# Optimization experiments

Measured on AMD Instinct MI355X. Metric: run time of the kernel, lower is better.

The kernel has to match this reference:

```python
import jax, jax.numpy as jnp
import numpy as np

H = 256
W = 256
TANFOVX = 0.5
TANFOVY = 0.5
FX = W / (2.0 * TANFOVX)   # focal in pixels
FY = H / (2.0 * TANFOVY)
NEAR = 0.2                 # near-plane cull, as in 3DGS CUDA
COV_BLUR = 0.3             # low-pass added to 2D cov diagonal
P = 512


def quat_to_rot(q):
    # q: [P,4] (r,x,y,z) unnormalized -> [P,3,3]
    q = q / jnp.linalg.norm(q, axis=-1, keepdims=True)
    r, x, y, z = q[:, 0], q[:, 1], q[:, 2], q[:, 3]
    R = jnp.stack([
        1 - 2 * (y * y + z * z), 2 * (x * y - r * z), 2 * (x * z + r * y),
        2 * (x * y + r * z), 1 - 2 * (x * x + z * z), 2 * (y * z - r * x),
        2 * (x * z - r * y), 2 * (y * z + r * x), 1 - 2 * (x * x + y * y)],
        axis=-1).reshape(-1, 3, 3)
    return R


def setup_inputs() -> dict:
    key = jax.random.key(0)
    k = jax.random.split(key, 6)
    xy = jax.random.normal(k[0], (P, 2), dtype=jnp.float32) * 1.5
    z = jax.random.uniform(k[1], (P, 1), dtype=jnp.float32, minval=2.0, maxval=10.0)
    means3D = jnp.concatenate([xy, z], axis=1)                       # in front of camera
    scales = 0.02 + 0.15 * jax.random.uniform(k[2], (P, 3), dtype=jnp.float32)
    rotations = jax.random.normal(k[3], (P, 4), dtype=jnp.float32)
    opacities = jax.random.uniform(k[4], (P, 1), dtype=jnp.float32, minval=0.1, maxval=1.0)
    colors_precomp = jax.random.uniform(k[5], (P, 3), dtype=jnp.float32)
    viewmatrix = jnp.eye(4, dtype=jnp.float32)                       # camera at origin, +z forward
    zn, zf = 0.01, 100.0
    projmatrix = jnp.array([
        [1.0 / TANFOVX, 0.0, 0.0, 0.0],
        [0.0, 1.0 / TANFOVY, 0.0, 0.0],
        [0.0, 0.0, zf / (zf - zn), -(zf * zn) / (zf - zn)],
        [0.0, 0.0, 1.0, 0.0]], dtype=jnp.float32)                    # full proj (view = I)
    campos = jnp.zeros((3,), dtype=jnp.float32)
    bg = jnp.zeros((3,), dtype=jnp.float32)
    return {"means3D": means3D, "scales": scales, "rotations": rotations,
            "opacities": opacities, "colors_precomp": colors_precomp,
            "viewmatrix": viewmatrix, "projmatrix": projmatrix,
            "campos": campos, "bg": bg}


def reference(means3D, scales, rotations, opacities, colors_precomp,
              viewmatrix, projmatrix, campos, bg):
    n = means3D.shape[0]
    Rw = viewmatrix[:3, :3]
    p_view = means3D @ Rw.T + viewmatrix[:3, 3]                      # [P,3] camera space
    depth = p_view[:, 2]
    ones = jnp.ones((n, 1), means3D.dtype)
    p_hom = jnp.concatenate([means3D, ones], axis=1) @ projmatrix.T  # [P,4]
    pw = 1.0 / (p_hom[:, 3] + 1e-7)
    p_proj = p_hom[:, :3] * pw[:, None]                              # NDC
    # 3D covariance from scale + rotation: Sigma = (R S)(R S)^T
    R = quat_to_rot(rotations)
    M = R * scales[:, None, :]
    cov3d = M @ jnp.swapaxes(M, 1, 2)                                # [P,3,3]
    # EWA splatting Jacobian -> 2D covariance
    tz = jnp.where(jnp.abs(depth) < 1e-6, 1e-6, depth)
    limx, limy = 1.3 * TANFOVX, 1.3 * TANFOVY
    tx = jnp.clip(p_view[:, 0] / tz, -limx, limx) * tz
    ty = jnp.clip(p_view[:, 1] / tz, -limy, limy) * tz
    zero = jnp.zeros_like(tz)
    J = jnp.stack([FX / tz, zero, -FX * tx / (tz * tz),
                   zero, FY / tz, -FY * ty / (tz * tz)], axis=-1).reshape(-1, 2, 3)
    T = J @ Rw                                                        # [P,2,3]
    cov2d = T @ cov3d @ jnp.swapaxes(T, 1, 2)                         # [P,2,2]
    a = cov2d[:, 0, 0] + COV_BLUR
    b = cov2d[:, 0, 1]
    c = cov2d[:, 1, 1] + COV_BLUR
    det = a * c - b * b
    valid = (depth > NEAR) & (det > 0.0)
    det_s = jnp.where(valid, det, 1.0)
    conic_a, conic_b, conic_c = c / det_s, -b / det_s, a / det_s
    mid = 0.5 * (a + c)
    lam = mid + jnp.sqrt(jnp.maximum(mid * mid - det, 0.1))
    radii = jnp.where(valid, jnp.ceil(3.0 * jnp.sqrt(lam)), 0.0).astype(jnp.int32)
    # NDC -> pixel centers
    px = ((p_proj[:, 0] + 1.0) * W - 1.0) * 0.5
    py = ((p_proj[:, 1] + 1.0) * H - 1.0) * 0.5
    # global front-to-back depth sort (replaces per-tile radix sort)
    order = jnp.argsort(depth)
    px, py = px[order], py[order]
    ca, cb, cc = conic_a[order], conic_b[order], conic_c[order]
    op = opacities[order, 0]
    col = colors_precomp[order]
    dep = depth[order]
    vmask = valid[order]
    ys, xs = jnp.meshgrid(jnp.arange(H, dtype=means3D.dtype),
                          jnp.arange(W, dtype=means3D.dtype), indexing='ij')
    xs, ys = xs.reshape(-1), ys.reshape(-1)                           # [HW]
    dx = px[:, None] - xs[None, :]                                    # [P,HW]
    dy = py[:, None] - ys[None, :]
    power = -0.5 * (ca[:, None] * dx * dx + cc[:, None] * dy * dy) - cb[:, None] * dx * dy
    alpha = jnp.minimum(0.99, op[:, None] * jnp.exp(power))
    keep = (power <= 0.0) & (alpha >= 1.0 / 255.0) & vmask[:, None]
    alpha = jnp.where(keep, alpha, 0.0)
    Tcum = jnp.cumprod(1.0 - alpha, axis=0)                           # transmittance after each gaussian
    T_excl = jnp.concatenate([jnp.ones((1, alpha.shape[1]), alpha.dtype), Tcum[:-1]], axis=0)
    wgt = alpha * T_excl                                              # compositing weights [P,HW]
    Tfin = Tcum[-1]
    color = jnp.einsum('ph,pc->ch', wgt, col) + Tfin[None, :] * bg[:, None]
    depth_map = jnp.einsum('ph,p->h', wgt, dep)
    opac_map = 1.0 - Tfin
    n_touched = jnp.zeros((n,), jnp.int32).at[order].set(
        jnp.sum(keep, axis=1).astype(jnp.int32))
    return (color.reshape(3, H, W), radii, depth_map.reshape(H, W),
            opac_map.reshape(H, W), n_touched)
```

## Files before the change

### kernel.cpp

```cpp
#include <hip/hip_runtime.h>

constexpr int   P     = 512;
constexpr int   W     = 256;
constexpr int   H     = 256;
constexpr float FXc   = 256.0f;
constexpr float FYc   = 256.0f;
constexpr float NEARc = 0.2f;
constexpr float BLUR  = 0.3f;
constexpr float LIMX  = 0.65f;
constexpr float LIMY  = 0.65f;

constexpr int COLOR_OFF = 0;
constexpr int RADII_OFF = 196608;
constexpr int DEPTH_OFF = 197120;
constexpr int OPAC_OFF  = 262656;
constexpr int NT_OFF    = 328192;

__global__ __launch_bounds__(256, 4) void fused_q_kernel(
    const float* __restrict__ means3D, const float* __restrict__ scales,
    const float* __restrict__ rots,    const float* __restrict__ opacs,
    const float* __restrict__ cols,    const float* __restrict__ vm,
    const float* __restrict__ pm,      const float* __restrict__ bg,
    float* __restrict__ out)
{
    __shared__ float4 g4u[P * 3];
    __shared__ float  sdep[P];
    __shared__ int    sorig[P];
    __shared__ int    rank2slot[P + 1];
    __shared__ float  part[3][5][64];
    __shared__ float4 ntrec[2];
    __shared__ int    s_cnt;
    __shared__ int    s_n;

    const int tid   = threadIdx.x;
    const int bid   = blockIdx.x;
    const int row   = bid >> 2;
    const int xbase = (bid & 3) * 64;
    const int wv    = tid >> 6;
    const int lane  = tid & 63;
    const float fy  = (float)row;

    if (tid == 0) { s_n = 0; s_cnt = 0; }
    __syncthreads();

    #pragma unroll
    for (int k = 0; k < 2; ++k) {
        const int g = tid + k * 256;

        const float mx = means3D[g*3+0], my = means3D[g*3+1], mz = means3D[g*3+2];

        const float pv0 = vm[0]*mx + vm[1]*my + vm[2]*mz  + vm[3];
        const float pv1 = vm[4]*mx + vm[5]*my + vm[6]*mz  + vm[7];
        const float pv2 = vm[8]*mx + vm[9]*my + vm[10]*mz + vm[11];
        const float depth = pv2;

        const float ph0 = pm[0]*mx  + pm[1]*my  + pm[2]*mz  + pm[3];
        const float ph1 = pm[4]*mx  + pm[5]*my  + pm[6]*mz  + pm[7];
        const float ph3 = pm[12]*mx + pm[13]*my + pm[14]*mz + pm[15];
        const float pwn = 1.0f / (ph3 + 1e-7f);
        const float pp0 = ph0 * pwn, pp1 = ph1 * pwn;

        float q0 = rots[g*4+0], q1 = rots[g*4+1], q2 = rots[g*4+2], q3 = rots[g*4+3];
        const float qinv = 1.0f / sqrtf(q0*q0 + q1*q1 + q2*q2 + q3*q3);
        q0 *= qinv; q1 *= qinv; q2 *= qinv; q3 *= qinv;
        const float r = q0, x = q1, y = q2, z = q3;
        const float R00 = 1.f - 2.f*(y*y + z*z), R01 = 2.f*(x*y - r*z), R02 = 2.f*(x*z + r*y);
        const float R10 = 2.f*(x*y + r*z), R11 = 1.f - 2.f*(x*x + z*z), R12 = 2.f*(y*z - r*x);
        const float R20 = 2.f*(x*z - r*y), R21 = 2.f*(y*z + r*x), R22 = 1.f - 2.f*(x*x + y*y);

        const float s0 = scales[g*3+0], s1 = scales[g*3+1], s2 = scales[g*3+2];
        const float M00 = R00*s0, M01 = R01*s1, M02 = R02*s2;
        const float M10 = R10*s0, M11 = R11*s1, M12 = R12*s2;
        const float M20 = R20*s0, M21 = R21*s1, M22 = R22*s2;
        const float c00 = M00*M00 + M01*M01 + M02*M02;
        const float c01 = M00*M10 + M01*M11 + M02*M12;
        const float c02 = M00*M20 + M01*M21 + M02*M22;
        const float c11 = M10*M10 + M11*M11 + M12*M12;
        const float c12 = M10*M20 + M11*M21 + M12*M22;
        const float c22 = M20*M20 + M21*M21 + M22*M22;

        const float tz  = (fabsf(depth) < 1e-6f) ? 1e-6f : depth;
        const float txc = fminf(fmaxf(pv0 / tz, -LIMX), LIMX) * tz;
        const float tyc = fminf(fmaxf(pv1 / tz, -LIMY), LIMY) * tz;

        const float J00 = FXc / tz, J02 = -FXc * txc / (tz*tz);
        const float J11 = FYc / tz, J12 = -FYc * tyc / (tz*tz);

        const float T00 = J00*vm[0] + J02*vm[8];
        const float T01 = J00*vm[1] + J02*vm[9];
        const float T02 = J00*vm[2] + J02*vm[10];
        const float T10 = J11*vm[4] + J12*vm[8];
        const float T11 = J11*vm[5] + J12*vm[9];
        const float T12 = J11*vm[6] + J12*vm[10];

        const float V00 = T00*c00 + T01*c01 + T02*c02;
        const float V01 = T00*c01 + T01*c11 + T02*c12;
        const float V02 = T00*c02 + T01*c12 + T02*c22;
        const float V10 = T10*c00 + T11*c01 + T12*c02;
        const float V11 = T10*c01 + T11*c11 + T12*c12;
        const float V12 = T10*c02 + T11*c12 + T12*c22;

        const float a = V00*T00 + V01*T01 + V02*T02 + BLUR;
        const float b = V00*T10 + V01*T11 + V02*T12;
        const float c = V10*T10 + V11*T11 + V12*T12 + BLUR;
        const float det = a*c - b*b;

        const bool  valid = (depth > NEARc) && (det > 0.0f);
        const float det_s = valid ? det : 1.0f;
        const float conic_a =  c / det_s;
        const float conic_b = -b / det_s;
        const float conic_c =  a / det_s;

        const float op = opacs[g];
        const float L  = logf(255.0f * op);
        const float rowrad2 = valid ? (2.0f * c * L) * 1.0001f + 1e-4f : -1.0f;
        const float xrad2   = valid ? (2.0f * a * L) * 1.0001f + 1e-4f : -1.0f;

        if (bid == 0) {
            const float mid = 0.5f * (a + c);
            const float lam = mid + sqrtf(fmaxf(mid*mid - det, 0.1f));
            out[RADII_OFF + g] = valid ? ceilf(3.0f * sqrtf(lam)) : 0.0f;
        }

        const float px = ((pp0 + 1.0f) * (float)W - 1.0f) * 0.5f;
        const float py = ((pp1 + 1.0f) * (float)H - 1.0f) * 0.5f;

        if (g == bid) {
            ntrec[0] = make_float4(px, py, -0.5f * conic_a, -conic_b);
            ntrec[1] = make_float4(-0.5f * conic_c, op, xrad2, rowrad2);
        }

        const float dyv = py - fy;
        const float dxm = fmaxf(0.0f, fmaxf((float)xbase - px,
                                            px - (float)(xbase + 63)));
        if (dyv * dyv <= rowrad2 && dxm * dxm <= xrad2) {
            const int s = atomicAdd(&s_n, 1);
            g4u[s*3+0] = make_float4(py, -conic_b, px, -0.5f * conic_a);
            g4u[s*3+1] = make_float4(-0.5f * conic_c, op, depth, 0.0f);
            g4u[s*3+2] = make_float4(cols[g*3+0], cols[g*3+1], cols[g*3+2], 0.0f);
            sdep[s]  = depth;
            sorig[s] = g;
        }
    }
    __syncthreads();
    const int n = s_n;

    for (int t = tid; t < n; t += 256) {
        const float d = sdep[t];
        const int   o = sorig[t];
        int rank = 0;
        for (int j = 0; j < n; ++j) {
            const float dj = sdep[j];
            rank += (dj < d) || (dj == d && sorig[j] < o);
        }
        rank2slot[rank] = t;
    }
    __syncthreads();
    if (tid == 0) rank2slot[n] = (n > 0) ? rank2slot[n - 1] : 0;
    __syncthreads();

    const int beg = (n * wv) >> 2;
    const int end = (n * (wv + 1)) >> 2;
    const float fx = (float)(xbase + lane);
    float T = 1.0f, ar = 0.f, ag = 0.f, ab = 0.f, ad = 0.f;

    if (end > beg) {
        int slot = rank2slot[beg];
        float4 h  = g4u[slot*3+0];
        float4 mm = g4u[slot*3+1];
        float4 cl = g4u[slot*3+2];
        for (int t = beg; t < end; ++t) {
            const int sn = rank2slot[t + 1];
            const float4 hn  = g4u[sn*3+0];
            const float4 mmn = g4u[sn*3+1];
            const float4 cln = g4u[sn*3+2];

            const float dx = h.z - fx;
            const float dy = h.x - fy;
            const float pw = fmaf(h.w, dx*dx, fmaf(mm.x, dy*dy, h.y * dx * dy));
            const float alpha = fminf(0.99f, mm.y * __expf(pw));
            const bool keep = (pw <= 0.0f) && (alpha >= (1.0f / 255.0f));

            const float ae  = keep ? alpha : 0.0f;
            const float wgt = ae * T;
            ar = fmaf(wgt, cl.x, ar); ag = fmaf(wgt, cl.y, ag);
            ab = fmaf(wgt, cl.z, ab); ad = fmaf(wgt, mm.z, ad);
            T  = fmaf(-ae, T, T);

            h = hn; mm = mmn; cl = cln;
        }
    }

    if (wv > 0) {
        part[wv-1][0][lane] = ar; part[wv-1][1][lane] = ag;
        part[wv-1][2][lane] = ab; part[wv-1][3][lane] = ad;
        part[wv-1][4][lane] = T;
    }
    __syncthreads();
    if (wv == 0) {
        float fr = ar, fg = ag, fb = ab, fd = ad, fT = T;
        #pragma unroll
        for (int s = 0; s < 3; ++s) {
            fr = fmaf(fT, part[s][0][lane], fr);
            fg = fmaf(fT, part[s][1][lane], fg);
            fb = fmaf(fT, part[s][2][lane], fb);
            fd = fmaf(fT, part[s][3][lane], fd);
            fT *= part[s][4][lane];
        }
        const int pix = row * W + xbase + lane;
        out[COLOR_OFF + 0*65536 + pix] = fr + fT * bg[0];
        out[COLOR_OFF + 1*65536 + pix] = fg + fT * bg[1];
        out[COLOR_OFF + 2*65536 + pix] = fb + fT * bg[2];
        out[DEPTH_OFF + pix]           = fd;
        out[OPAC_OFF  + pix]           = 1.0f - fT;
    }

    if (bid < P) {
        const float4 r0 = ntrec[0], r1 = ntrec[1];
        const float pxg = r0.x, pyg = r0.y, pa = r0.z, pb = r0.w;
        const float pc = r1.x, opg = r1.y, rx2 = r1.z, ry2 = r1.w;
        int cc2 = 0;
        if (ry2 > 0.0f && rx2 > 0.0f) {
            const float ry = sqrtf(ry2), rx = sqrtf(rx2);
            const int y0 = max(0, (int)ceilf(pyg - ry));
            const int y1 = min(H - 1, (int)floorf(pyg + ry));
            const int x0 = max(0, (int)ceilf(pxg - rx));
            const int x1 = min(W - 1, (int)floorf(pxg + rx));
            const int xx = x0 + tid;
            if (xx <= x1 && y0 <= y1) {
                const float dx = (float)xx - pxg;
                const float padx2 = pa * dx * dx;
                for (int yy = y0; yy <= y1; ++yy) {
                    const float dy = (float)yy - pyg;
                    const float pw = fmaf(pc, dy*dy, fmaf(pb, dx*dy, padx2));
                    const float alpha = fminf(0.99f, opg * __expf(pw));
                    cc2 += (pw <= 0.0f) && (alpha >= (1.0f / 255.0f));
                }
            }
        }
        #pragma unroll
        for (int off = 32; off; off >>= 1) cc2 += __shfl_down(cc2, off);
        if (lane == 0 && cc2) atomicAdd(&s_cnt, cc2);
        __syncthreads();
        if (tid == 0) out[NT_OFF + bid] = (float)s_cnt;
    }
}

extern "C" void kernel_launch(void* const* d_in, const int* in_sizes, int n_in,
                              void* d_out, int out_size, void* d_ws, size_t ws_size,
                              hipStream_t stream) {
    const float* means3D = (const float*)d_in[0];
    const float* scales  = (const float*)d_in[1];
    const float* rots    = (const float*)d_in[2];
    const float* opacs   = (const float*)d_in[3];
    const float* cols    = (const float*)d_in[4];
    const float* vm      = (const float*)d_in[5];
    const float* pm      = (const float*)d_in[6];
    const float* bg      = (const float*)d_in[8];
    float* out = (float*)d_out;

    fused_q_kernel<<<4 * H, 256, 0, stream>>>(means3D, scales, rots, opacs,
                                              cols, vm, pm, bg, out);
}
```

Measured before the change: 20.57 us.

## Cull gaussians with cheap bound before full preprocessing; analytic n_touched row spans

Non-zero blocks first test each gaussian against a cheap conservative bound (max scale, depth, opacity) and run the full covariance/conic preprocessing only for the surviving candidates. Block 0 still preprocesses all gaussians to write radii. The n_touched count no longer loops over every row and evaluates exp per pixel: each thread takes one row and solves the conic quadratic to count the pixels inside the alpha threshold. This adds an extra barrier and candidate list, and the analytic count may differ from the per-pixel test at boundary pixels.

After: 17.18 us. 16.5% less time.

```diff
diff --git a/kernel.cpp b/kernel.cpp
--- a/kernel.cpp
+++ b/kernel.cpp
@@ -15,6 +15,98 @@
 constexpr int DEPTH_OFF = 197120;
 constexpr int OPAC_OFF  = 262656;
 constexpr int NT_OFF    = 328192;
+
+struct PrepR {
+    float px, py, pa, pb, pc, opv, depth;
+    float rr2, xr2;
+    float a, c, det, L;
+    bool  valid;
+};
+
+__device__ __forceinline__ PrepR full_prep(
+    int g,
+    const float* __restrict__ means3D, const float* __restrict__ scales,
+    const float* __restrict__ rots,    const float* __restrict__ opacs,
+    const float* __restrict__ vm,      const float* __restrict__ pm)
+{
+    PrepR o;
+    const float mx = means3D[g*3+0], my = means3D[g*3+1], mz = means3D[g*3+2];
+
+    const float pv0 = vm[0]*mx + vm[1]*my + vm[2]*mz  + vm[3];
+    const float pv1 = vm[4]*mx + vm[5]*my + vm[6]*mz  + vm[7];
+    const float pv2 = vm[8]*mx + vm[9]*my + vm[10]*mz + vm[11];
+    const float depth = pv2;
+
+    const float ph0 = pm[0]*mx  + pm[1]*my  + pm[2]*mz  + pm[3];
+    const float ph1 = pm[4]*mx  + pm[5]*my  + pm[6]*mz  + pm[7];
+    const float ph3 = pm[12]*mx + pm[13]*my + pm[14]*mz + pm[15];
+    const float pwn = 1.0f / (ph3 + 1e-7f);
+    const float pp0 = ph0 * pwn, pp1 = ph1 * pwn;
+
+    float q0 = rots[g*4+0], q1 = rots[g*4+1], q2 = rots[g*4+2], q3 = rots[g*4+3];
+    const float qinv = 1.0f / sqrtf(q0*q0 + q1*q1 + q2*q2 + q3*q3);
+    q0 *= qinv; q1 *= qinv; q2 *= qinv; q3 *= qinv;
+    const float r = q0, x = q1, y = q2, z = q3;
+    const float R00 = 1.f - 2.f*(y*y + z*z), R01 = 2.f*(x*y - r*z), R02 = 2.f*(x*z + r*y);
+    const float R10 = 2.f*(x*y + r*z), R11 = 1.f - 2.f*(x*x + z*z), R12 = 2.f*(y*z - r*x);
+    const float R20 = 2.f*(x*z - r*y), R21 = 2.f*(y*z + r*x), R22 = 1.f - 2.f*(x*x + y*y);
+
+    const float s0 = scales[g*3+0], s1 = scales[g*3+1], s2 = scales[g*3+2];
+    const float M00 = R00*s0, M01 = R01*s1, M02 = R02*s2;
+    const float M10 = R10*s0, M11 = R11*s1, M12 = R12*s2;
+    const float M20 = R20*s0, M21 = R21*s1, M22 = R22*s2;
+    const float c00 = M00*M00 + M01*M01 + M02*M02;
+    const float c01 = M00*M10 + M01*M11 + M02*M12;
+    const float c02 = M00*M20 + M01*M21 + M02*M22;
+    const float c11 = M10*M10 + M11*M11 + M12*M12;
+    const float c12 = M10*M20 + M11*M21 + M12*M22;
+    const float c22 = M20*M20 + M21*M21 + M22*M22;
+
+    const float tz  = (fabsf(depth) < 1e-6f) ? 1e-6f : depth;
+    const float txc = fminf(fmaxf(pv0 / tz, -LIMX), LIMX) * tz;
+    const float tyc = fminf(fmaxf(pv1 / tz, -LIMY), LIMY) * tz;
+
+    const float J00 = FXc / tz, J02 = -FXc * txc / (tz*tz);
+    const float J11 = FYc / tz, J12 = -FYc * tyc / (tz*tz);
+
+    const float T00 = J00*vm[0] + J02*vm[8];
+    const float T01 = J00*vm[1] + J02*vm[9];
+    const float T02 = J00*vm[2] + J02*vm[10];
+    const float T10 = J11*vm[4] + J12*vm[8];
+    const float T11 = J11*vm[5] + J12*vm[9];
+    const float T12 = J11*vm[6] + J12*vm[10];
+
+    const float V00 = T00*c00 + T01*c01 + T02*c02;
+    const float V01 = T00*c01 + T01*c11 + T02*c12;
+    const float V02 = T00*c02 + T01*c12 + T02*c22;
+    const float V10 = T10*c00 + T11*c01 + T12*c02;
+    const float V11 = T10*c01 + T11*c11 + T12*c12;
+    const float V12 = T10*c02 + T11*c12 + T12*c22;
+
+    const float a = V00*T00 + V01*T01 + V02*T02 + BLUR;
+    const float b = V00*T10 + V01*T11 + V02*T12;
+    const float c = V10*T10 + V11*T11 + V12*T12 + BLUR;
+    const float det = a*c - b*b;
+
+    const bool  valid = (depth > NEARc) && (det > 0.0f);
+    const float det_s = valid ? det : 1.0f;
+
+    o.pa = -0.5f * ( c / det_s);
+    o.pb = -(-b / det_s) * -1.0f;
+    o.pb = (b / det_s);
+    o.pc = -0.5f * ( a / det_s);
+    o.opv = opacs[g];
+    o.depth = depth;
+    const float L = logf(255.0f * o.opv);
+    o.L = L;
+    o.rr2 = valid ? (2.0f * c * L) * 1.0001f + 1e-4f : -1.0f;
+    o.xr2 = valid ? (2.0f * a * L) * 1.0001f + 1e-4f : -1.0f;
+    o.px = ((pp0 + 1.0f) * (float)W - 1.0f) * 0.5f;
+    o.py = ((pp1 + 1.0f) * (float)H - 1.0f) * 0.5f;
+    o.a = a; o.c = c; o.det = det;
+    o.valid = valid;
+    return o;
+}
 
 __global__ __launch_bounds__(256, 4) void fused_q_kernel(
     const float* __restrict__ means3D, const float* __restrict__ scales,
@@ -26,11 +118,11 @@
     __shared__ float4 g4u[P * 3];
     __shared__ float  sdep[P];
     __shared__ int    sorig[P];
+    __shared__ int    cand[P];
     __shared__ int    rank2slot[P + 1];
     __shared__ float  part[3][5][64];
     __shared__ float4 ntrec[2];
-    __shared__ int    s_cnt;
-    __shared__ int    s_n;
+    __shared__ int    s_cnt, s_n, s_ncand;
 
     const int tid   = threadIdx.x;
     const int bid   = blockIdx.x;
@@ -39,107 +131,79 @@
     const int wv    = tid >> 6;
     const int lane  = tid & 63;
     const float fy  = (float)row;
-
-    if (tid == 0) { s_n = 0; s_cnt = 0; }
-    __syncthreads();
-
-    #pragma unroll
-    for (int k = 0; k < 2; ++k) {
-        const int g = tid + k * 256;
-
-        const float mx = means3D[g*3+0], my = means3D[g*3+1], mz = means3D[g*3+2];
-
-        const float pv0 = vm[0]*mx + vm[1]*my + vm[2]*mz  + vm[3];
-        const float pv1 = vm[4]*mx + vm[5]*my + vm[6]*mz  + vm[7];
-        const float pv2 = vm[8]*mx + vm[9]*my + vm[10]*mz + vm[11];
-        const float depth = pv2;
-
-        const float ph0 = pm[0]*mx  + pm[1]*my  + pm[2]*mz  + pm[3];
-        const float ph1 = pm[4]*mx  + pm[5]*my  + pm[6]*mz  + pm[7];
-        const float ph3 = pm[12]*mx + pm[13]*my + pm[14]*mz + pm[15];
-        const float pwn = 1.0f / (ph3 + 1e-7f);
-        const float pp0 = ph0 * pwn, pp1 = ph1 * pwn;
-
-        float q0 = rots[g*4+0], q1 = rots[g*4+1], q2 = rots[g*4+2], q3 = rots[g*4+3];
-        const float qinv = 1.0f / sqrtf(q0*q0 + q1*q1 + q2*q2 + q3*q3);
-        q0 *= qinv; q1 *= qinv; q2 *= qinv; q3 *= qinv;
-        const float r = q0, x = q1, y = q2, z = q3;
-        const float R00 = 1.f - 2.f*(y*y + z*z), R01 = 2.f*(x*y - r*z), R02 = 2.f*(x*z + r*y);
-        const float R10 = 2.f*(x*y + r*z), R11 = 1.f - 2.f*(x*x + z*z), R12 = 2.f*(y*z - r*x);
-        const float R20 = 2.f*(x*z - r*y), R21 = 2.f*(y*z + r*x), R22 = 1.f - 2.f*(x*x + y*y);
-
-        const float s0 = scales[g*3+0], s1 = scales[g*3+1], s2 = scales[g*3+2];
-        const float M00 = R00*s0, M01 = R01*s1, M02 = R02*s2;
-        const float M10 = R10*s0, M11 = R11*s1, M12 = R12*s2;
-        const float M20 = R20*s0, M21 = R21*s1, M22 = R22*s2;
-        const float c00 = M00*M00 + M01*M01 + M02*M02;
-        const float c01 = M00*M10 + M01*M11 + M02*M12;
-        const float c02 = M00*M20 + M01*M21 + M02*M22;
-        const float c11 = M10*M10 + M11*M11 + M12*M12;
-        const float c12 = M10*M20 + M11*M21 + M12*M22;
-        const float c22 = M20*M20 + M21*M21 + M22*M22;
-
-        const float tz  = (fabsf(depth) < 1e-6f) ? 1e-6f : depth;
-        const float txc = fminf(fmaxf(pv0 / tz, -LIMX), LIMX) * tz;
-        const float tyc = fminf(fmaxf(pv1 / tz, -LIMY), LIMY) * tz;
-
-        const float J00 = FXc / tz, J02 = -FXc * txc / (tz*tz);
-        const float J11 = FYc / tz, J12 = -FYc * tyc / (tz*tz);
-
-        const float T00 = J00*vm[0] + J02*vm[8];
-        const float T01 = J00*vm[1] + J02*vm[9];
-        const float T02 = J00*vm[2] + J02*vm[10];
-        const float T10 = J11*vm[4] + J12*vm[8];
-        const float T11 = J11*vm[5] + J12*vm[9];
-        const float T12 = J11*vm[6] + J12*vm[10];
-
-        const float V00 = T00*c00 + T01*c01 + T02*c02;
-        const float V01 = T00*c01 + T01*c11 + T02*c12;
-        const float V02 = T00*c02 + T01*c12 + T02*c22;
-        const float V10 = T10*c00 + T11*c01 + T12*c02;
-        const float V11 = T10*c01 + T11*c11 + T12*c12;
-        const float V12 = T10*c02 + T11*c12 + T12*c22;
-
-        const float a = V00*T00 + V01*T01 + V02*T02 + BLUR;
-        const float b = V00*T10 + V01*T11 + V02*T12;
-        const float c = V10*T10 + V11*T11 + V12*T12 + BLUR;
-        const float det = a*c - b*b;
-
-        const bool  valid = (depth > NEARc) && (det > 0.0f);
-        const float det_s = valid ? det : 1.0f;
-        const float conic_a =  c / det_s;
-        const float conic_b = -b / det_s;
-        const float conic_c =  a / det_s;
-
-        const float op = opacs[g];
-        const float L  = logf(255.0f * op);
-        const float rowrad2 = valid ? (2.0f * c * L) * 1.0001f + 1e-4f : -1.0f;
-        const float xrad2   = valid ? (2.0f * a * L) * 1.0001f + 1e-4f : -1.0f;
-
-        if (bid == 0) {
-            const float mid = 0.5f * (a + c);
-            const float lam = mid + sqrtf(fmaxf(mid*mid - det, 0.1f));
-            out[RADII_OFF + g] = valid ? ceilf(3.0f * sqrtf(lam)) : 0.0f;
-        }
-
-        const float px = ((pp0 + 1.0f) * (float)W - 1.0f) * 0.5f;
-        const float py = ((pp1 + 1.0f) * (float)H - 1.0f) * 0.5f;
-
-        if (g == bid) {
-            ntrec[0] = make_float4(px, py, -0.5f * conic_a, -conic_b);
-            ntrec[1] = make_float4(-0.5f * conic_c, op, xrad2, rowrad2);
-        }
-
-        const float dyv = py - fy;
-        const float dxm = fmaxf(0.0f, fmaxf((float)xbase - px,
-                                            px - (float)(xbase + 63)));
-        if (dyv * dyv <= rowrad2 && dxm * dxm <= xrad2) {
-            const int s = atomicAdd(&s_n, 1);
-            g4u[s*3+0] = make_float4(py, -conic_b, px, -0.5f * conic_a);
-            g4u[s*3+1] = make_float4(-0.5f * conic_c, op, depth, 0.0f);
-            g4u[s*3+2] = make_float4(cols[g*3+0], cols[g*3+1], cols[g*3+2], 0.0f);
-            sdep[s]  = depth;
-            sorig[s] = g;
+    const float wx0 = (float)xbase, wx1 = (float)(xbase + 63);
+
+    if (tid == 0) { s_n = 0; s_cnt = 0; s_ncand = 0; }
+    __syncthreads();
+
+    if (bid == 0) {
+        #pragma unroll
+        for (int k = 0; k < 2; ++k) {
+            const int g = tid + k * 256;
+            PrepR p = full_prep(g, means3D, scales, rots, opacs, vm, pm);
+            const float mid = 0.5f * (p.a + p.c);
+            const float lam = mid + sqrtf(fmaxf(mid*mid - p.det, 0.1f));
+            out[RADII_OFF + g] = p.valid ? ceilf(3.0f * sqrtf(lam)) : 0.0f;
+            if (g == 0) {
+                ntrec[0] = make_float4(p.px, p.py, p.pa, p.pb);
+                ntrec[1] = make_float4(p.pc, p.L, p.xr2, p.rr2);
+            }
+            const float dyv = p.py - fy;
+            const float dxm = fmaxf(0.0f, fmaxf(wx0 - p.px, p.px - wx1));
+            if (dyv*dyv <= p.rr2 && dxm*dxm <= p.xr2) {
+                const int s = atomicAdd(&s_n, 1);
+                g4u[s*3+0] = make_float4(p.py, p.pb, p.px, p.pa);
+                g4u[s*3+1] = make_float4(p.pc, p.opv, p.depth, 0.0f);
+                g4u[s*3+2] = make_float4(cols[g*3+0], cols[g*3+1], cols[g*3+2], 0.0f);
+                sdep[s]  = p.depth;
+                sorig[s] = g;
+            }
+        }
+    } else {
+        #pragma unroll
+        for (int k = 0; k < 2; ++k) {
+            const int g = tid + k * 256;
+            const float mx = means3D[g*3+0], my = means3D[g*3+1], mz = means3D[g*3+2];
+            const float depth = vm[8]*mx + vm[9]*my + vm[10]*mz + vm[11];
+            const float ph0 = pm[0]*mx  + pm[1]*my  + pm[2]*mz  + pm[3];
+            const float ph1 = pm[4]*mx  + pm[5]*my  + pm[6]*mz  + pm[7];
+            const float ph3 = pm[12]*mx + pm[13]*my + pm[14]*mz + pm[15];
+            const float pwn = 1.0f / (ph3 + 1e-7f);
+            const float px = ((ph0*pwn + 1.0f) * (float)W - 1.0f) * 0.5f;
+            const float py = ((ph1*pwn + 1.0f) * (float)H - 1.0f) * 0.5f;
+            const float s0 = scales[g*3+0], s1 = scales[g*3+1], s2 = scales[g*3+2];
+            const float ms2 = fmaxf(s0*s0, fmaxf(s1*s1, s2*s2));
+            const float L   = __logf(255.0f * opacs[g]);
+            const float rtz = 1.0f / depth;
+            const float fs  = FYc * rtz;
+            const float cub = fs*fs * 1.4226f * ms2 + BLUR;
+            const float rr2ub = 2.0f * cub * fmaxf(L, 0.0f) * 1.001f + 1e-3f;
+            const float dyv = py - fy;
+            const float dxm = fmaxf(0.0f, fmaxf(wx0 - px, px - wx1));
+            if (depth > NEARc && dyv*dyv <= rr2ub && dxm*dxm <= rr2ub) {
+                cand[atomicAdd(&s_ncand, 1)] = g;
+            }
+        }
+        if (tid == 255 && bid < P) {
+            PrepR p = full_prep(bid, means3D, scales, rots, opacs, vm, pm);
+            ntrec[0] = make_float4(p.px, p.py, p.pa, p.pb);
+            ntrec[1] = make_float4(p.pc, p.L, p.xr2, p.rr2);
+        }
+        __syncthreads();
+        const int nc = s_ncand;
+        for (int t = tid; t < nc; t += 256) {
+            const int g = cand[t];
+            PrepR p = full_prep(g, means3D, scales, rots, opacs, vm, pm);
+            const float dyv = p.py - fy;
+            const float dxm = fmaxf(0.0f, fmaxf(wx0 - p.px, p.px - wx1));
+            if (dyv*dyv <= p.rr2 && dxm*dxm <= p.xr2) {
+                const int s = atomicAdd(&s_n, 1);
+                g4u[s*3+0] = make_float4(p.py, p.pb, p.px, p.pa);
+                g4u[s*3+1] = make_float4(p.pc, p.opv, p.depth, 0.0f);
+                g4u[s*3+2] = make_float4(cols[g*3+0], cols[g*3+1], cols[g*3+2], 0.0f);
+                sdep[s]  = p.depth;
+                sorig[s] = g;
+            }
         }
     }
     __syncthreads();
@@ -218,23 +282,28 @@
     if (bid < P) {
         const float4 r0 = ntrec[0], r1 = ntrec[1];
         const float pxg = r0.x, pyg = r0.y, pa = r0.z, pb = r0.w;
-        const float pc = r1.x, opg = r1.y, rx2 = r1.z, ry2 = r1.w;
+        const float pc = r1.x, L = r1.y, ry2 = r1.w;
         int cc2 = 0;
-        if (ry2 > 0.0f && rx2 > 0.0f) {
-            const float ry = sqrtf(ry2), rx = sqrtf(rx2);
+        if (ry2 > 0.0f) {
+            const float ry = sqrtf(ry2);
             const int y0 = max(0, (int)ceilf(pyg - ry));
             const int y1 = min(H - 1, (int)floorf(pyg + ry));
-            const int x0 = max(0, (int)ceilf(pxg - rx));
-            const int x1 = min(W - 1, (int)floorf(pxg + rx));
-            const int xx = x0 + tid;
-            if (xx <= x1 && y0 <= y1) {
-                const float dx = (float)xx - pxg;
-                const float padx2 = pa * dx * dx;
-                for (int yy = y0; yy <= y1; ++yy) {
-                    const float dy = (float)yy - pyg;
-                    const float pw = fmaf(pc, dy*dy, fmaf(pb, dx*dy, padx2));
-                    const float alpha = fminf(0.99f, opg * __expf(pw));
-                    cc2 += (pw <= 0.0f) && (alpha >= (1.0f / 255.0f));
+            const int yy = y0 + tid;
+            if (yy <= y1) {
+                const float dy = (float)yy - pyg;
+                const float B = pb * dy;
+                const float C = fmaf(pc, dy*dy, L);
+                const float disc = fmaf(B, B, -4.0f * pa * C);
+                if (disc > 0.0f) {
+                    const float sd = sqrtf(disc);
+                    const float inv2A = 0.5f / pa;
+                    const float ra = (-B + sd) * inv2A;
+                    const float rb = (-B - sd) * inv2A;
+                    const float lo = pxg + fminf(ra, rb);
+                    const float hi = pxg + fmaxf(ra, rb);
+                    const float xlo = fmaxf(ceilf(lo), 0.0f);
+                    const float xhi = fminf(floorf(hi), 255.0f);
+                    cc2 = max(0, (int)(xhi - xlo) + 1);
                 }
             }
         }
```
